# Kernel tuning notes

Measured on AMD Instinct MI355X. Metric: run time of the kernel, lower is better.

The kernel has to match this reference:

```python
import jax, jax.numpy as jnp
import numpy as np

N_HEAD, N_KV, HEAD_DIM, GATE_CH = 16, 4, 128, 32

def _rope(x, cos, sin):
    d = x.shape[3] // 2
    x1, x2 = x[..., :d], x[..., d:]
    return jnp.concatenate([x1 * cos + x2 * sin, x1 * (-sin) + x2 * cos], axis=3)

def _rmsnorm(x):
    xf = x.astype(jnp.float32)
    return (x * jax.lax.rsqrt(jnp.mean(xf * xf, axis=-1, keepdims=True) + 1e-6)).astype(x.dtype)

def setup_inputs() -> dict:
    key = jax.random.key(0)
    ks = jax.random.split(key, 9)
    B, T, C = 2, 2048, 2048
    return {
        "x":  jax.random.normal(ks[0], (B, T, C), jnp.float32),
        "ve": jax.random.normal(ks[1], (B, T, N_KV * HEAD_DIM), jnp.float32),
        "cos": jax.random.uniform(ks[2], (T, 1, HEAD_DIM // 2), jnp.float32),
        "sin": jax.random.uniform(ks[3], (T, 1, HEAD_DIM // 2), jnp.float32),
        "Wq": jax.random.normal(ks[4], (C, N_HEAD * HEAD_DIM), jnp.float32) * 0.02,
        "Wk": jax.random.normal(ks[5], (C, N_KV * HEAD_DIM), jnp.float32) * 0.02,
        "Wv": jax.random.normal(ks[6], (C, N_KV * HEAD_DIM), jnp.float32) * 0.02,
        "Wg": jax.random.normal(ks[7], (GATE_CH, N_KV), jnp.float32) * 0.02,
        "Wo": jax.random.normal(ks[8], (C, C), jnp.float32) * 0.02,
        "window": 1024,
    }

def reference(x, ve, cos, sin, Wq, Wk, Wv, Wg, Wo, window):
    B, T, C = x.shape
    q = (x @ Wq).reshape(B, T, N_HEAD, HEAD_DIM)
    k = (x @ Wk).reshape(B, T, N_KV, HEAD_DIM)
    v = (x @ Wv).reshape(B, T, N_KV, HEAD_DIM)
    # value-embedding gate (ve_gate active for this layer)
    gate = 2.0 * jax.nn.sigmoid(x[..., :GATE_CH] @ Wg)  # (B,T,N_KV)
    v = v + gate[..., None] * ve.reshape(B, T, N_KV, HEAD_DIM)
    q, k = _rope(q, cos, sin), _rope(k, cos, sin)
    q, k = _rmsnorm(q), _rmsnorm(k)
    # GQA: repeat kv heads (repeat_interleave over head dim)
    groups = N_HEAD // N_KV
    k = jnp.repeat(k, groups, axis=2)
    v = jnp.repeat(v, groups, axis=2)
    scale = 1.0 / np.sqrt(HEAD_DIM)
    scores = jnp.einsum("bthd,bshd->bhts", q, k) * scale  # (B,H,T,T)
    idx = jnp.arange(T)
    diff = idx[None, :] - idx[:, None]  # diff[i,j] = j - i, as in torch code
    mask = (diff >= 0) & (diff < window)
    scores = jnp.where(mask[None, None], scores, -jnp.inf)
    p = jax.nn.softmax(scores, axis=-1)
    y = jnp.einsum("bhts,bshd->bthd", p, v).reshape(B, T, C)
    return y @ Wo
```

## Files before the change

kernel.cpp:

```cpp
#include <hip/hip_runtime.h>
#include <hip/hip_bf16.h>
#include <cstdint>

typedef __hip_bfloat16 bf16;
typedef __attribute__((ext_vector_type(8))) short short8;
typedef __attribute__((ext_vector_type(4))) short short4v;
typedef __attribute__((ext_vector_type(4))) float f32x4;

#define T_   2048
#define CDIM 2048
#define NH   16
#define NKV  4
#define HD   128
#define QSCALE (0.08838834764831845f * 1.44269504088896340f)

__device__ __forceinline__ void gload_lds16(const void* g, void* l) {
  __builtin_amdgcn_global_load_lds(
      (const __attribute__((address_space(1))) void*)g,
      (__attribute__((address_space(3))) void*)l, 16, 0, 0);
}

template <int G> __device__ __forceinline__ void vm_gate() {
  if constexpr (G == 6)      asm volatile("s_waitcnt vmcnt(6)" ::: "memory");
  else if constexpr (G == 5) asm volatile("s_waitcnt vmcnt(5)" ::: "memory");
  else                       asm volatile("s_waitcnt vmcnt(0)" ::: "memory");
}

__global__ __launch_bounds__(256) void cast_x_kernel(const float4* __restrict__ in,
                                                     ushort4* __restrict__ out, int n4) {
  int i = blockIdx.x * 256 + threadIdx.x;
  if (i >= n4) return;
  float4 v = in[i];
  union { bf16 h[4]; ushort4 u; } cv;
  cv.h[0] = __float2bfloat16(v.x);
  cv.h[1] = __float2bfloat16(v.y);
  cv.h[2] = __float2bfloat16(v.z);
  cv.h[3] = __float2bfloat16(v.w);
  out[i] = cv.u;
}

__global__ __launch_bounds__(256) void cast_transpose(const float* __restrict__ W,
                                                      bf16* __restrict__ WT,
                                                      int K, int N) {
  __shared__ float tile[32][33];
  int k0 = blockIdx.y * 32, n0 = blockIdx.x * 32;
  int r = threadIdx.x >> 5, c = threadIdx.x & 31;
  for (int i = 0; i < 4; ++i)
    tile[r + i * 8][c] = W[(size_t)(k0 + r + i * 8) * N + n0 + c];
  __syncthreads();
  for (int i = 0; i < 4; ++i)
    WT[(size_t)(n0 + r + i * 8) * K + k0 + c] = __float2bfloat16(tile[c][r + i * 8]);
}

template <int MREP, int NREP, typename CT>
__global__ __launch_bounds__(512, 2) void gemm_pp(const bf16* __restrict__ A,
                                                  const bf16* __restrict__ BT,
                                                  CT* __restrict__ C,
                                                  int N, int K, int RY, int RX) {
  constexpr int BM = MREP * 32;
  constexpr int BN = NREP * 64;
  constexpr int QN = (MREP == 8) ? 4 : 2;
  constexpr int MI = MREP / 4;
  constexpr int GATE = NREP + QN - 1;
  __shared__ __align__(16) bf16 sA[2][BM * 64];
  __shared__ __align__(16) bf16 sB[2][BN * 64];

  int tid = threadIdx.x;
  int lane = tid & 63, w = tid >> 6;
  int wm = w >> 2, wn = w & 3;
  int lr = lane & 15, lk = lane >> 4;

  int xcd = blockIdx.x & 7, t = blockIdx.x >> 3;
  int by = (xcd >> 1) * RY + t / RX;
  int bx = (xcd & 1) * RX + t % RX;
  int m0 = by * BM, n0 = bx * BN;

  f32x4 acc[MREP][NREP];
#pragma unroll
  for (int m = 0; m < MREP; ++m)
#pragma unroll
    for (int n = 0; n < NREP; ++n) acc[m][n] = (f32x4){0.f, 0.f, 0.f, 0.f};

  const bf16* Abase = A + (size_t)m0 * K;
  const bf16* Bbase = BT + (size_t)n0 * K;

  auto stageB = [&](int p, int kt) {
    int kb = kt << 6;
#pragma unroll
    for (int i = 0; i < NREP; ++i) {
      int c = i * 512 + tid;
      int r = c >> 3, sl = c & 7;
      gload_lds16(Bbase + (size_t)r * K + kb + ((sl ^ (r & 7)) << 3),
                  (char*)(&sB[p][0]) + c * 16);
    }
  };
  auto stageAq = [&](int p, int kt, int q) {
    int kb = kt << 6;
    int rbase = 32 * q + ((w & 3) << 3) + ((w >> 2) * (BM / 2));
    int r = rbase + (lane >> 3), sl = lane & 7;
    gload_lds16(Abase + (size_t)r * K + kb + ((sl ^ (r & 7)) << 3),
                (char*)(&sA[p][0]) + rbase * 128 + lane * 16);
  };

  int nk = K >> 6;
  stageB(0, 0);
#pragma unroll
  for (int q = 0; q < QN; ++q) stageAq(0, 0, q);
  stageB(1, 1);
#pragma unroll
  for (int q = 0; q < QN - 1; ++q) stageAq(1, 1, q);
  vm_gate<GATE>();
  __builtin_amdgcn_s_barrier();

#define READ_A_FRAGS(PH)                                                   \
  {                                                                        \
    _Pragma("unroll")                                                      \
    for (int mi = 0; mi < MI; ++mi) {                                      \
      int row = wm * (MREP * 16) + ((PH) * MI + mi) * 16 + lr;             \
      const char* rb = sAb + row * 128;                                    \
      int rx = (row & 7) << 4;                                             \
      af[mi][0] = *(const short8*)(rb + ((lk * 16) ^ rx));                 \
      af[mi][1] = *(const short8*)(rb + ((64 + lk * 16) ^ rx));            \
    }                                                                      \
  }
#define MFMA_PH(PH)                                                        \
  __builtin_amdgcn_s_setprio(1);                                           \
  _Pragma("unroll")                                                        \
  for (int kk = 0; kk < 2; ++kk)                                           \
    _Pragma("unroll")                                                      \
    for (int mi = 0; mi < MI; ++mi)                                        \
      _Pragma("unroll")                                                    \
      for (int n = 0; n < NREP; ++n)                                       \
        acc[(PH) * MI + mi][n] = __builtin_amdgcn_mfma_f32_16x16x32_bf16(  \
            af[mi][kk], bfr[n][kk], acc[(PH) * MI + mi][n], 0, 0, 0);      \
  __builtin_amdgcn_s_setprio(0);
#define WAIT_LGKM                                                          \
  asm volatile("s_waitcnt lgkmcnt(0)" ::: "memory");                       \
  __builtin_amdgcn_sched_barrier(0);

  for (int kt = 0; kt < nk; ++kt) {
    int p = kt & 1;
    const char* sAb = (const char*)(&sA[p][0]);
    const char* sBb = (const char*)(&sB[p][0]);
    short8 bfr[NREP][2], af[MI][2];

#pragma unroll
    for (int n = 0; n < NREP; ++n) {
      int row = wn * (NREP * 16) + n * 16 + lr;
      const char* rb = sBb + row * 128;
      int rx = (row & 7) << 4;
      bfr[n][0] = *(const short8*)(rb + ((lk * 16) ^ rx));
      bfr[n][1] = *(const short8*)(rb + ((64 + lk * 16) ^ rx));
    }
    READ_A_FRAGS(0);
    if (kt + 1 < nk) stageAq(p ^ 1, kt + 1, QN - 1);
    __builtin_amdgcn_s_barrier();
    WAIT_LGKM;
    MFMA_PH(0);
    __builtin_amdgcn_s_barrier();

    READ_A_FRAGS(1);
    if (kt + 2 < nk) {
      stageB(p, kt + 2);
      if constexpr (QN == 4) stageAq(p, kt + 2, 0);
    }
    __builtin_amdgcn_s_barrier();
    WAIT_LGKM;
    MFMA_PH(1);
    __builtin_amdgcn_s_barrier();

    READ_A_FRAGS(2);
    if (kt + 2 < nk) stageAq(p, kt + 2, (QN == 4) ? 1 : 0);
    __builtin_amdgcn_s_barrier();
    WAIT_LGKM;
    MFMA_PH(2);
    __builtin_amdgcn_s_barrier();

    READ_A_FRAGS(3);
    if constexpr (QN == 4) {
      if (kt + 2 < nk) stageAq(p, kt + 2, 2);
    }
    __builtin_amdgcn_s_barrier();
    WAIT_LGKM;
    MFMA_PH(3);
    if (kt + 2 < nk) vm_gate<GATE>();
    else             vm_gate<0>();
    __builtin_amdgcn_s_barrier();
  }
#undef READ_A_FRAGS
#undef MFMA_PH
#undef WAIT_LGKM

#pragma unroll
  for (int m = 0; m < MREP; ++m)
#pragma unroll
    for (int n = 0; n < NREP; ++n)
#pragma unroll
      for (int jj = 0; jj < 4; ++jj) {
        size_t idx = (size_t)(m0 + wm * (MREP * 16) + m * 16 + lk * 4 + jj) * N +
                     n0 + wn * (NREP * 16) + n * 16 + lr;
        if constexpr (__is_same(CT, float))
          C[idx] = acc[m][n][jj];
        else
          C[idx] = __float2bfloat16(acc[m][n][jj]);
      }
}

__global__ __launch_bounds__(256) void epilogue_kernel(
    const bf16* __restrict__ qkv, const float* __restrict__ x,
    const float* __restrict__ ve, const float* __restrict__ cosT,
    const float* __restrict__ sinT, const float* __restrict__ Wg,
    bf16* __restrict__ qn, bf16* __restrict__ kn, bf16* __restrict__ vT) {
  int row = blockIdx.x;
  int bi = row >> 11, t = row & 2047;
  int tid = threadIdx.x, lane = tid & 63, w = tid >> 6;
  __shared__ float gate[NKV];
  size_t rb = (size_t)row * 3072;

  if (tid < 128) {
    int g = tid >> 5, i = tid & 31;
    float p = x[(size_t)row * CDIM + i] * Wg[i * 4 + g];
    p += __shfl_xor(p, 1);  p += __shfl_xor(p, 2);
    p += __shfl_xor(p, 4);  p += __shfl_xor(p, 8);
    p += __shfl_xor(p, 16);
    if (i == 0) gate[g] = 2.f / (1.f + __expf(-p));
  }
  __syncthreads();

  float cv = cosT[t * 64 + lane];
  float sv = sinT[t * 64 + lane];

  for (int it = 0; it < 4; ++it) {
    int h = it * 4 + w;
    float x1 = __bfloat162float(qkv[rb + h * 128 + lane]);
    float x2 = __bfloat162float(qkv[rb + h * 128 + 64 + lane]);
    float y1 = x1 * cv + x2 * sv;
    float y2 = x2 * cv - x1 * sv;
    float ss = y1 * y1 + y2 * y2;
    ss += __shfl_xor(ss, 1);  ss += __shfl_xor(ss, 2);  ss += __shfl_xor(ss, 4);
    ss += __shfl_xor(ss, 8);  ss += __shfl_xor(ss, 16); ss += __shfl_xor(ss, 32);
    float r = rsqrtf(ss * (1.f / 128.f) + 1e-6f) * QSCALE;
    size_t ob = (size_t)row * (NH * HD) + h * 128;
    qn[ob + lane] = __float2bfloat16(y1 * r);
    qn[ob + 64 + lane] = __float2bfloat16(y2 * r);
  }
  {
    int h = w;
    float x1 = __bfloat162float(qkv[rb + 2048 + h * 128 + lane]);
    float x2 = __bfloat162float(qkv[rb + 2048 + h * 128 + 64 + lane]);
    float y1 = x1 * cv + x2 * sv;
    float y2 = x2 * cv - x1 * sv;
    float ss = y1 * y1 + y2 * y2;
    ss += __shfl_xor(ss, 1);  ss += __shfl_xor(ss, 2);  ss += __shfl_xor(ss, 4);
    ss += __shfl_xor(ss, 8);  ss += __shfl_xor(ss, 16); ss += __shfl_xor(ss, 32);
    float r = rsqrtf(ss * (1.f / 128.f) + 1e-6f);
    size_t ob = (size_t)row * (NKV * HD) + h * 128;
    kn[ob + lane] = __float2bfloat16(y1 * r);
    kn[ob + 64 + lane] = __float2bfloat16(y2 * r);
  }
  for (int e = tid; e < 512; e += 256) {
    int kv = e >> 7, d = e & 127;
    float val = __bfloat162float(qkv[rb + 2560 + e]) + gate[kv] * ve[(size_t)row * 512 + e];
    vT[((size_t)(bi * NKV + kv) * HD + d) * T_ + t] = __float2bfloat16(val);
  }
}

__global__ __launch_bounds__(256, 2) void attn_kernel(
    const bf16* __restrict__ qn, const bf16* __restrict__ kn,
    const bf16* __restrict__ vT, bf16* __restrict__ y,
    const int* __restrict__ winp) {
  __shared__ __align__(16) bf16 sK[64 * 128];
  __shared__ __align__(16) bf16 sV[128 * 64];

  int win = *winp;
  int id = blockIdx.x;
  int g  = id & 7;
  int bi = g >> 2, kvh = g & 3;
  int rem = id >> 3;
  int h  = kvh * 4 + (rem & 3);
  int q0 = (rem >> 2) << 7;
  int tid = threadIdx.x;
  int lane = tid & 63, w = tid >> 6;
  int lr = lane & 15, lk = lane >> 4;

  short8 qfA[4], qfB[4];
  {
    const bf16* qrA = qn + (size_t)(bi * T_ + q0 + w * 32 + lr) * (NH * HD) + h * HD;
    const bf16* qrB = qrA + (size_t)16 * (NH * HD);
#pragma unroll
    for (int c = 0; c < 4; ++c) {
      qfA[c] = *(const short8*)(qrA + c * 32 + lk * 8);
      qfB[c] = *(const short8*)(qrB + c * 32 + lk * 8);
    }
  }

  int kge[4], klb[4], vge[4], vlbA[4], vlbB[4];
#pragma unroll
  for (int i = 0; i < 4; ++i) {
    int c = i * 256 + tid;
    int kr = c >> 4, ks = c & 15;
    kge[i] = kr * (NKV * HD) + ks * 8;
    klb[i] = kr * 256 + ((ks ^ (kr & 7)) << 4);
    int vr = c >> 3, vs = c & 7;
    vge[i] = vr * T_ + vs * 8;
    int hh = vs >> 2, m = vs & 3, a = m >> 1;
    int sA = 8 * ((2 * m) & 3) + 4 * a;
    int sB = 8 * ((2 * m + 1) & 3) + 4 * a;
    int tA = 64 * hh + 2 * sA, tB = 64 * hh + 2 * sB;
    vlbA[i] = vr * 128 + (((tA >> 4) ^ (vr & 7)) << 4) + (tA & 15);
    vlbB[i] = vr * 128 + (((tB >> 4) ^ (vr & 7)) << 4) + (tB & 15);
  }
  const bf16* kpane = kn + (size_t)bi * T_ * (NKV * HD) + kvh * HD;
  const bf16* vpane = vT + (size_t)(bi * NKV + kvh) * HD * T_;

  short8 kreg[4], vreg[4];
  auto LOAD = [&](int jtx) {
    const bf16* kb = kpane + (size_t)(jtx << 6) * (NKV * HD);
    const bf16* vb = vpane + (jtx << 6);
#pragma unroll
    for (int i = 0; i < 4; ++i) kreg[i] = *(const short8*)(kb + kge[i]);
#pragma unroll
    for (int i = 0; i < 4; ++i) vreg[i] = *(const short8*)(vb + vge[i]);
  };
  auto WRITE = [&]() {
#pragma unroll
    for (int i = 0; i < 4; ++i) *(short8*)((char*)sK + klb[i]) = kreg[i];
#pragma unroll
    for (int i = 0; i < 4; ++i) {
      union { short8 s8; short4v s4[2]; } u;
      u.s8 = vreg[i];
      *(short4v*)((char*)sV + vlbA[i]) = u.s4[0];
      *(short4v*)((char*)sV + vlbB[i]) = u.s4[1];
    }
  };

  f32x4 o0[8], o1[8];
#pragma unroll
  for (int i = 0; i < 8; ++i) {
    o0[i] = (f32x4){0.f, 0.f, 0.f, 0.f};
    o1[i] = (f32x4){0.f, 0.f, 0.f, 0.f};
  }
  float lp0 = 0.f, lp1 = 0.f;

  int jt0 = q0 >> 6;
  int hi = q0 + 126 + win; if (hi > T_ - 1) hi = T_ - 1;
  int jt1 = hi >> 6;

  LOAD(jt0);
  WRITE();
  if (jt0 < jt1) LOAD(jt0 + 1);
  asm volatile("s_waitcnt lgkmcnt(0)\n\ts_barrier" ::: "memory");

  int irow0 = q0 + w * 32 + lr;
  int klo = lk * 4;

  for (int jt = jt0; jt <= jt1; ++jt) {
    int j0 = jt << 6;

    f32x4 s0[4], s1[4];
#pragma unroll
    for (int sub = 0; sub < 4; ++sub) {
      s0[sub] = (f32x4){0.f, 0.f, 0.f, 0.f};
      s1[sub] = (f32x4){0.f, 0.f, 0.f, 0.f};
    }
    __builtin_amdgcn_s_setprio(1);
#pragma unroll
    for (int sub = 0; sub < 4; ++sub) {
      int kr = sub * 16 + lr;
      int rx = (kr & 7) << 4;
      const char* rowb = (const char*)sK + kr * 256;
#pragma unroll
      for (int c = 0; c < 4; ++c) {
        short8 kf = *(const short8*)(rowb + ((c * 64 + lk * 16) ^ rx));
        s0[sub] = __builtin_amdgcn_mfma_f32_16x16x32_bf16(kf, qfA[c], s0[sub], 0, 0, 0);
        s1[sub] = __builtin_amdgcn_mfma_f32_16x16x32_bf16(kf, qfB[c], s1[sub], 0, 0, 0);
      }
    }
    __builtin_amdgcn_s_setprio(0);

    bool full = (j0 >= q0 + 128) && (j0 + 64 <= q0 + win);
    int koff0 = j0 - irow0;
    int koff1 = koff0 - 16;

    short8 pA0, pA1, pB0, pB1;
    {
      unsigned pk[8];
#pragma unroll
      for (int sub = 0; sub < 4; ++sub) {
        float p0 = exp2f(s0[sub][0]), p1 = exp2f(s0[sub][1]);
        float p2 = exp2f(s0[sub][2]), p3 = exp2f(s0[sub][3]);
        if (!full) {
          int base = koff0 + sub * 16 + klo;
          p0 = ((unsigned)(base + 0) < (unsigned)win) ? p0 : 0.f;
          p1 = ((unsigned)(base + 1) < (unsigned)win) ? p1 : 0.f;
          p2 = ((unsigned)(base + 2) < (unsigned)win) ? p2 : 0.f;
          p3 = ((unsigned)(base + 3) < (unsigned)win) ? p3 : 0.f;
        }
        lp0 += (p0 + p1) + (p2 + p3);
        asm("v_cvt_pk_bf16_f32 %0, %1, %2" : "=v"(pk[sub * 2])     : "v"(p0), "v"(p1));
        asm("v_cvt_pk_bf16_f32 %0, %1, %2" : "=v"(pk[sub * 2 + 1]) : "v"(p2), "v"(p3));
      }
      union { unsigned u[4]; short8 s8; } c0, c1;
      c0.u[0] = pk[0]; c0.u[1] = pk[1]; c0.u[2] = pk[2]; c0.u[3] = pk[3];
      c1.u[0] = pk[4]; c1.u[1] = pk[5]; c1.u[2] = pk[6]; c1.u[3] = pk[7];
      pA0 = c0.s8; pA1 = c1.s8;
    }
    {
      unsigned pk[8];
#pragma unroll
      for (int sub = 0; sub < 4; ++sub) {
        float p0 = exp2f(s1[sub][0]), p1 = exp2f(s1[sub][1]);
        float p2 = exp2f(s1[sub][2]), p3 = exp2f(s1[sub][3]);
        if (!full) {
          int base = koff1 + sub * 16 + klo;
          p0 = ((unsigned)(base + 0) < (unsigned)win) ? p0 : 0.f;
          p1 = ((unsigned)(base + 1) < (unsigned)win) ? p1 : 0.f;
          p2 = ((unsigned)(base + 2) < (unsigned)win) ? p2 : 0.f;
          p3 = ((unsigned)(base + 3) < (unsigned)win) ? p3 : 0.f;
        }
        lp1 += (p0 + p1) + (p2 + p3);
        asm("v_cvt_pk_bf16_f32 %0, %1, %2" : "=v"(pk[sub * 2])     : "v"(p0), "v"(p1));
        asm("v_cvt_pk_bf16_f32 %0, %1, %2" : "=v"(pk[sub * 2 + 1]) : "v"(p2), "v"(p3));
      }
      union { unsigned u[4]; short8 s8; } c0, c1;
      c0.u[0] = pk[0]; c0.u[1] = pk[1]; c0.u[2] = pk[2]; c0.u[3] = pk[3];
      c1.u[0] = pk[4]; c1.u[1] = pk[5]; c1.u[2] = pk[6]; c1.u[3] = pk[7];
      pB0 = c0.s8; pB1 = c1.s8;
    }

    __builtin_amdgcn_s_setprio(1);
#pragma unroll
    for (int nb = 0; nb < 8; ++nb) {
      int vr = nb * 16 + lr;
      int vrx = (vr & 7) << 4;
      const char* vb = (const char*)sV + vr * 128;
      short8 vf0 = *(const short8*)(vb + ((lk * 16) ^ vrx));
      short8 vf1 = *(const short8*)(vb + ((64 + lk * 16) ^ vrx));
      o0[nb] = __builtin_amdgcn_mfma_f32_16x16x32_bf16(pA0, vf0, o0[nb], 0, 0, 0);
      o0[nb] = __builtin_amdgcn_mfma_f32_16x16x32_bf16(pA1, vf1, o0[nb], 0, 0, 0);
      o1[nb] = __builtin_amdgcn_mfma_f32_16x16x32_bf16(pB0, vf0, o1[nb], 0, 0, 0);
      o1[nb] = __builtin_amdgcn_mfma_f32_16x16x32_bf16(pB1, vf1, o1[nb], 0, 0, 0);
    }
    __builtin_amdgcn_s_setprio(0);

    asm volatile("s_waitcnt lgkmcnt(0)\n\ts_barrier" ::: "memory");
    if (jt < jt1) {
      WRITE();
      if (jt + 1 < jt1) LOAD(jt + 2);
      asm volatile("s_waitcnt lgkmcnt(0)\n\ts_barrier" ::: "memory");
    }
  }

  float l0 = lp0, l1 = lp1;
  l0 += __shfl_xor(l0, 16); l0 += __shfl_xor(l0, 32);
  l1 += __shfl_xor(l1, 16); l1 += __shfl_xor(l1, 32);
#pragma unroll
  for (int jj = 0; jj < 4; ++jj) {
    float inv0 = 1.f / __shfl(l0, klo + jj);
    float inv1 = 1.f / __shfl(l1, klo + jj);
    size_t ob0 = (size_t)(bi * T_ + q0 + w * 32 + klo + jj) * (NH * HD) + h * HD;
    size_t ob1 = ob0 + (size_t)16 * (NH * HD);
#pragma unroll
    for (int nb = 0; nb < 8; ++nb) {
      y[ob0 + nb * 16 + lr] = __float2bfloat16(o0[nb][jj] * inv0);
      y[ob1 + nb * 16 + lr] = __float2bfloat16(o1[nb][jj] * inv1);
    }
  }
}

extern "C" void kernel_launch(void* const* d_in, const int* in_sizes, int n_in,
                              void* d_out, int out_size, void* d_ws, size_t ws_size,
                              hipStream_t stream) {
  const float* x    = (const float*)d_in[0];
  const float* ve   = (const float*)d_in[1];
  const float* cosT = (const float*)d_in[2];
  const float* sinT = (const float*)d_in[3];
  const float* Wq   = (const float*)d_in[4];
  const float* Wk   = (const float*)d_in[5];
  const float* Wv   = (const float*)d_in[6];
  const float* Wg   = (const float*)d_in[7];
  const float* Wo   = (const float*)d_in[8];
  const int*   win  = (const int*)d_in[9];
  float* out = (float*)d_out;

  char* ws = (char*)d_ws;
  bf16*  xb   = (bf16*)(ws);
  bf16*  wT   = (bf16*)(ws + 16777216);
  bf16*  woT  = (bf16*)(ws + 29360128);
  bf16*  qkvb = (bf16*)(ws + 37748736);
  bf16*  qn   = (bf16*)(ws + 62914560);
  bf16*  kn   = (bf16*)(ws + 79691776);
  bf16*  vTb  = (bf16*)(ws + 83886080);
  bf16*  y    = qkvb;

  cast_x_kernel<<<8192, 256, 0, stream>>>((const float4*)x, (ushort4*)xb, 2097152);
  cast_transpose<<<dim3(64, 64), 256, 0, stream>>>(Wq, wT, 2048, 2048);
  cast_transpose<<<dim3(16, 64), 256, 0, stream>>>(Wk, wT + (size_t)2048 * 2048, 2048, 512);
  cast_transpose<<<dim3(16, 64), 256, 0, stream>>>(Wv, wT + (size_t)2560 * 2048, 2048, 512);
  cast_transpose<<<dim3(64, 64), 256, 0, stream>>>(Wo, woT, 2048, 2048);

  gemm_pp<8, 3, bf16><<<256, 512, 0, stream>>>(xb, wT, qkvb, 3072, 2048, 4, 8);
  epilogue_kernel<<<4096, 256, 0, stream>>>(qkvb, x, ve, cosT, sinT, Wg, qn, kn, vTb);
  attn_kernel<<<512, 256, 0, stream>>>(qn, kn, vTb, y, win);
  gemm_pp<4, 4, float><<<256, 512, 0, stream>>>(y, woT, out, 2048, 2048, 8, 4);
}
```

Baseline: 195.6 us.

## Double-buffer attention K/V tiles in LDS and drop pre-MFMA GEMM barriers

The attention kernel now keeps two LDS buffers for the K and V tiles. The next tile is written into the idle buffer at the start of each iteration, while compute reads the current one, and only one wait-plus-barrier remains per iteration instead of two. Separately, the GEMM main loop drops the workgroup barrier before each MFMA phase and keeps only the per-wave LDS-count wait, which relies on the barrier after each phase to order buffer reuse. The trade-off is twice the attention LDS footprint, which could limit occupancy, and a correctness dependence on the remaining barriers covering the GEMM staging hazards.

```diff
diff --git a/kernel.cpp b/kernel.cpp
--- a/kernel.cpp
+++ b/kernel.cpp
@@ -134,7 +134,7 @@
         acc[(PH) * MI + mi][n] = __builtin_amdgcn_mfma_f32_16x16x32_bf16(  \
             af[mi][kk], bfr[n][kk], acc[(PH) * MI + mi][n], 0, 0, 0);      \
   __builtin_amdgcn_s_setprio(0);
-#define WAIT_LGKM                                                          \
+#define LGKM_FENCE                                                         \
   asm volatile("s_waitcnt lgkmcnt(0)" ::: "memory");                       \
   __builtin_amdgcn_sched_barrier(0);
 
@@ -154,8 +154,7 @@
     }
     READ_A_FRAGS(0);
     if (kt + 1 < nk) stageAq(p ^ 1, kt + 1, QN - 1);
-    __builtin_amdgcn_s_barrier();
-    WAIT_LGKM;
+    LGKM_FENCE;
     MFMA_PH(0);
     __builtin_amdgcn_s_barrier();
 
@@ -164,15 +163,13 @@
       stageB(p, kt + 2);
       if constexpr (QN == 4) stageAq(p, kt + 2, 0);
     }
-    __builtin_amdgcn_s_barrier();
-    WAIT_LGKM;
+    LGKM_FENCE;
     MFMA_PH(1);
     __builtin_amdgcn_s_barrier();
 
     READ_A_FRAGS(2);
     if (kt + 2 < nk) stageAq(p, kt + 2, (QN == 4) ? 1 : 0);
-    __builtin_amdgcn_s_barrier();
-    WAIT_LGKM;
+    LGKM_FENCE;
     MFMA_PH(2);
     __builtin_amdgcn_s_barrier();
 
@@ -180,8 +177,7 @@
     if constexpr (QN == 4) {
       if (kt + 2 < nk) stageAq(p, kt + 2, 2);
     }
-    __builtin_amdgcn_s_barrier();
-    WAIT_LGKM;
+    LGKM_FENCE;
     MFMA_PH(3);
     if (kt + 2 < nk) vm_gate<GATE>();
     else             vm_gate<0>();
@@ -189,7 +185,7 @@
   }
 #undef READ_A_FRAGS
 #undef MFMA_PH
-#undef WAIT_LGKM
+#undef LGKM_FENCE
 
 #pragma unroll
   for (int m = 0; m < MREP; ++m)
@@ -269,8 +265,8 @@
     const bf16* __restrict__ qn, const bf16* __restrict__ kn,
     const bf16* __restrict__ vT, bf16* __restrict__ y,
     const int* __restrict__ winp) {
-  __shared__ __align__(16) bf16 sK[64 * 128];
-  __shared__ __align__(16) bf16 sV[128 * 64];
+  __shared__ __align__(16) bf16 sK[2][64 * 128];
+  __shared__ __align__(16) bf16 sV[2][128 * 64];
 
   int win = *winp;
   int id = blockIdx.x;
@@ -322,15 +318,17 @@
 #pragma unroll
     for (int i = 0; i < 4; ++i) vreg[i] = *(const short8*)(vb + vge[i]);
   };
-  auto WRITE = [&]() {
-#pragma unroll
-    for (int i = 0; i < 4; ++i) *(short8*)((char*)sK + klb[i]) = kreg[i];
+  auto WRITE = [&](int b) {
+    char* kBuf = (char*)(&sK[b][0]);
+    char* vBuf = (char*)(&sV[b][0]);
+#pragma unroll
+    for (int i = 0; i < 4; ++i) *(short8*)(kBuf + klb[i]) = kreg[i];
 #pragma unroll
     for (int i = 0; i < 4; ++i) {
       union { short8 s8; short4v s4[2]; } u;
       u.s8 = vreg[i];
-      *(short4v*)((char*)sV + vlbA[i]) = u.s4[0];
-      *(short4v*)((char*)sV + vlbB[i]) = u.s4[1];
+      *(short4v*)(vBuf + vlbA[i]) = u.s4[0];
+      *(short4v*)(vBuf + vlbB[i]) = u.s4[1];
     }
   };
 
@@ -347,15 +345,24 @@
   int jt1 = hi >> 6;
 
   LOAD(jt0);
-  WRITE();
+  WRITE(0);
   if (jt0 < jt1) LOAD(jt0 + 1);
   asm volatile("s_waitcnt lgkmcnt(0)\n\ts_barrier" ::: "memory");
 
   int irow0 = q0 + w * 32 + lr;
   int klo = lk * 4;
 
+  int p = 0;
   for (int jt = jt0; jt <= jt1; ++jt) {
     int j0 = jt << 6;
+
+    if (jt < jt1) {
+      WRITE(p ^ 1);
+      if (jt + 1 < jt1) LOAD(jt + 2);
+    }
+
+    const char* sKb = (const char*)(&sK[p][0]);
+    const char* sVb = (const char*)(&sV[p][0]);
 
     f32x4 s0[4], s1[4];
 #pragma unroll
@@ -368,7 +375,7 @@
     for (int sub = 0; sub < 4; ++sub) {
       int kr = sub * 16 + lr;
       int rx = (kr & 7) << 4;
-      const char* rowb = (const char*)sK + kr * 256;
+      const char* rowb = sKb + kr * 256;
 #pragma unroll
       for (int c = 0; c < 4; ++c) {
         short8 kf = *(const short8*)(rowb + ((c * 64 + lk * 16) ^ rx));
@@ -433,7 +440,7 @@
     for (int nb = 0; nb < 8; ++nb) {
       int vr = nb * 16 + lr;
       int vrx = (vr & 7) << 4;
-      const char* vb = (const char*)sV + vr * 128;
+      const char* vb = sVb + vr * 128;
       short8 vf0 = *(const short8*)(vb + ((lk * 16) ^ vrx));
       short8 vf1 = *(const short8*)(vb + ((64 + lk * 16) ^ vrx));
       o0[nb] = __builtin_amdgcn_mfma_f32_16x16x32_bf16(pA0, vf0, o0[nb], 0, 0, 0);
@@ -444,11 +451,7 @@
     __builtin_amdgcn_s_setprio(0);
 
     asm volatile("s_waitcnt lgkmcnt(0)\n\ts_barrier" ::: "memory");
-    if (jt < jt1) {
-      WRITE();
-      if (jt + 1 < jt1) LOAD(jt + 2);
-      asm volatile("s_waitcnt lgkmcnt(0)\n\ts_barrier" ::: "memory");
-    }
+    p ^= 1;
   }
 
   float l0 = lp0, l1 = lp1;
```

After: 193.4 us. Within noise of the previous version (-1.1%).
